# Kernel tuning notes

Hardware: AMD Instinct MI355X
Metric: run time of the kernel (lower is better)

Reference implementation:

```python
import jax, jax.numpy as jnp
import numpy as np

H = 16      # query heads
KV = 8      # kv heads
D = 128     # head_dim
HID = 2048  # hidden_size
T = 2048    # tokens
EPS = 1e-6
THETA = 1000000.0


def setup_inputs() -> dict:
    key = jax.random.key(0)
    ks = jax.random.split(key, 4)
    return {
        "hidden_states": jax.random.normal(ks[0], (T, HID), jnp.float32),
        "positions": jnp.arange(T, dtype=jnp.int32),
        "qkv_w": jax.random.normal(ks[1], (H * D + 2 * KV * D, HID), jnp.float32) * 0.02,
        "o_w": jax.random.normal(ks[2], (HID, H * D), jnp.float32) * 0.02,
        "q_norm_w": jnp.ones((D,), jnp.float32),
        "k_norm_w": jnp.ones((D,), jnp.float32),
    }


def _rmsnorm(x, w):
    # x: [T, heads, D]; normalize over last dim
    var = jnp.mean(x * x, axis=-1, keepdims=True)
    return x * jax.lax.rsqrt(var + EPS) * w


def _rope(x, positions):
    # neox-style rotate-half; x: [T, heads, D]
    half = D // 2
    inv_freq = 1.0 / (THETA ** (jnp.arange(0, half, dtype=jnp.float32) / half * 1.0))
    inv_freq = 1.0 / (THETA ** (jnp.arange(0, D, 2, dtype=jnp.float32) / D))
    ang = positions.astype(jnp.float32)[:, None] * inv_freq  # [T, D/2]
    cos = jnp.cos(ang)[:, None, :]
    sin = jnp.sin(ang)[:, None, :]
    x1, x2 = x[..., :half], x[..., half:]
    return jnp.concatenate([x1 * cos - x2 * sin, x2 * cos + x1 * sin], axis=-1)


def reference(hidden_states, positions, qkv_w, o_w, q_norm_w, k_norm_w):
    scale = D ** -0.5
    qkv = hidden_states @ qkv_w.T  # [T, H*D + 2*KV*D]
    q = qkv[:, : H * D].reshape(T, H, D)
    k = qkv[:, H * D : H * D + KV * D].reshape(T, KV, D)
    v = qkv[:, H * D + KV * D :].reshape(T, KV, D)

    q = _rope(_rmsnorm(q, q_norm_w), positions)
    k = _rope(_rmsnorm(k, k_norm_w), positions)

    # GQA: repeat kv heads to match query heads
    rep = H // KV
    k = jnp.repeat(k, rep, axis=1)  # [T, H, D]
    v = jnp.repeat(v, rep, axis=1)

    scores = jnp.einsum("thd,shd->hts", q, k) * scale  # [H, T, T]
    causal = positions[:, None] >= positions[None, :]  # [T, T]
    scores = jnp.where(causal[None, :, :], scores, jnp.float32(-1e30))
    p = jax.nn.softmax(scores, axis=-1)
    o = jnp.einsum("hts,shd->thd", p, v).reshape(T, H * D)
    return o @ o_w.T  # [T, HID]
```

## Files before the change

### kernel.cpp

```cpp
#include <hip/hip_runtime.h>
#include <math.h>

#define T_TOK 2048
#define HID 2048
#define NH 16
#define NKV 8
#define HD 128
#define QKV_N 4096
#define EPS 1e-6f

typedef unsigned short u16;
typedef unsigned int   u32;
typedef __attribute__((ext_vector_type(8))) u16   u16x8;
typedef __attribute__((ext_vector_type(8))) short short8;
typedef __attribute__((ext_vector_type(4))) float floatx4;
typedef __attribute__((ext_vector_type(4))) u32   u32x4;

__device__ __forceinline__ u16 f2bf(float x) {
    u32 u = __float_as_uint(x);
    u = (u + 0x7fffu + ((u >> 16) & 1u)) >> 16;
    return (u16)u;
}
__device__ __forceinline__ float bf2f(u16 h) {
    return __uint_as_float(((u32)h) << 16);
}

__global__ __launch_bounds__(256) void cvt_f32_bf16(
    const float* __restrict__ in, u16* __restrict__ out)
{
    const size_t i = ((size_t)blockIdx.x * 256 + threadIdx.x) * 8;
    float4 a = *(const float4*)(in + i);
    float4 b = *(const float4*)(in + i + 4);
    u16x8 o;
    o[0] = f2bf(a.x); o[1] = f2bf(a.y); o[2] = f2bf(a.z); o[3] = f2bf(a.w);
    o[4] = f2bf(b.x); o[5] = f2bf(b.y); o[6] = f2bf(b.z); o[7] = f2bf(b.w);
    *(u16x8*)(out + i) = o;
}

template<bool OUT_BF16>
__global__ __launch_bounds__(256) void gemm_bt_bf16(
    const u16* __restrict__ A, const u16* __restrict__ B,
    void* __restrict__ Cv, int K, int lda, int ldb, int ldc)
{
    __shared__ short As[128 * 32];
    __shared__ short Bs[128 * 32];

    const int tid = threadIdx.x;
    const int w   = tid >> 6;
    const int l   = tid & 63;
    const int m0  = blockIdx.y * 128;
    const int n0  = blockIdx.x * 128;
    const int wm  = (w >> 1) * 64;
    const int wn  = (w & 1) * 64;
    const int lm  = l & 15;
    const int ko8 = (l >> 4) * 8;

    const u16* gA0 = A + (size_t)(m0      + (tid >> 2)) * lda + (tid & 3) * 8;
    const u16* gA1 = A + (size_t)(m0 + 64 + (tid >> 2)) * lda + (tid & 3) * 8;
    const u16* gB0 = B + (size_t)(n0      + (tid >> 2)) * ldb + (tid & 3) * 8;
    const u16* gB1 = B + (size_t)(n0 + 64 + (tid >> 2)) * ldb + (tid & 3) * 8;
    short* lA0 = As + w * 512;
    short* lA1 = As + 2048 + w * 512;
    short* lB0 = Bs + w * 512;
    short* lB1 = Bs + 2048 + w * 512;

    floatx4 acc[4][4];
    #pragma unroll
    for (int i = 0; i < 4; ++i)
        #pragma unroll
        for (int j = 0; j < 4; ++j) acc[i][j] = (floatx4){0.f, 0.f, 0.f, 0.f};

    for (int k0 = 0; k0 < K; k0 += 32) {
        __syncthreads();
        __builtin_amdgcn_global_load_lds(
            (const __attribute__((address_space(1))) u32*)(gA0 + k0),
            (__attribute__((address_space(3))) u32*)lA0, 16, 0, 0);
        __builtin_amdgcn_global_load_lds(
            (const __attribute__((address_space(1))) u32*)(gA1 + k0),
            (__attribute__((address_space(3))) u32*)lA1, 16, 0, 0);
        __builtin_amdgcn_global_load_lds(
            (const __attribute__((address_space(1))) u32*)(gB0 + k0),
            (__attribute__((address_space(3))) u32*)lB0, 16, 0, 0);
        __builtin_amdgcn_global_load_lds(
            (const __attribute__((address_space(1))) u32*)(gB1 + k0),
            (__attribute__((address_space(3))) u32*)lB1, 16, 0, 0);
        __syncthreads();

        short8 af[4], bfr[4];
        #pragma unroll
        for (int i = 0; i < 4; ++i)
            af[i] = *(const short8*)(As + (wm + i * 16 + lm) * 32 + ko8);
        #pragma unroll
        for (int j = 0; j < 4; ++j)
            bfr[j] = *(const short8*)(Bs + (wn + j * 16 + lm) * 32 + ko8);
        #pragma unroll
        for (int i = 0; i < 4; ++i)
            #pragma unroll
            for (int j = 0; j < 4; ++j)
                acc[i][j] = __builtin_amdgcn_mfma_f32_16x16x32_bf16(
                    af[i], bfr[j], acc[i][j], 0, 0, 0);
    }

    const int r0 = (l >> 4) * 4;
    #pragma unroll
    for (int i = 0; i < 4; ++i)
        #pragma unroll
        for (int j = 0; j < 4; ++j)
            #pragma unroll
            for (int r = 0; r < 4; ++r) {
                const int row = m0 + wm + i * 16 + r0 + r;
                const int col = n0 + wn + j * 16 + lm;
                if (OUT_BF16)
                    ((u16*)Cv)[(size_t)row * ldc + col] = f2bf(acc[i][j][r]);
                else
                    ((float*)Cv)[(size_t)row * ldc + col] = acc[i][j][r];
            }
}

__global__ __launch_bounds__(128) void norm_rope(
    u16* __restrict__ qkv, const int* __restrict__ positions,
    const float* __restrict__ qw, const float* __restrict__ kw)
{
    const int t   = blockIdx.x;
    const int hh  = blockIdx.y;
    const int tid = threadIdx.x;

    u16* p; const float* w;
    if (hh < NH) { p = qkv + (size_t)t*QKV_N + hh*HD;              w = qw; }
    else         { p = qkv + (size_t)t*QKV_N + NH*HD + (hh-NH)*HD; w = kw; }

    float x = bf2f(p[tid]);

    __shared__ float red[2];
    float ss = x * x;
    #pragma unroll
    for (int o = 32; o > 0; o >>= 1) ss += __shfl_down(ss, o);
    if ((tid & 63) == 0) red[tid >> 6] = ss;
    __syncthreads();
    const float var = (red[0] + red[1]) * (1.0f / (float)HD);
    float xn = x * rsqrtf(var + EPS) * w[tid];

    __shared__ float sx[HD];
    sx[tid] = xn;
    __syncthreads();

    const int   pos = positions[t];
    const int   i   = tid & 63;
    const float inv_freq = exp2f(-(float)i * 0.311430758895690f);
    const float ang = (float)pos * inv_freq;
    const float s = sinf(ang);
    const float c = cosf(ang);

    float out;
    if (tid < 64) out = sx[i]      * c - sx[i + 64] * s;
    else          out = sx[i + 64] * c + sx[i]      * s;
    p[tid] = f2bf(out);
}

__global__ __launch_bounds__(256) void k_pack(
    const u16* __restrict__ qkv, u16* __restrict__ Kp)
{
    const int tile = blockIdx.x, kvh = blockIdx.y, tid = threadIdx.x;
    const int r  = tid >> 2;
    const int og = (tid & 3) * 4;
    const u16* src = qkv + (size_t)(tile*64 + r)*QKV_N + NH*HD + kvh*HD;
    u16* dst = Kp + ((size_t)(kvh*32 + tile)*64 + r) * 128;
    #pragma unroll
    for (int i = 0; i < 4; ++i) {
        const int o = og + i;
        *(u16x8*)(dst + o*8) = *(const u16x8*)(src + (o ^ (r & 15))*8);
    }
}

__global__ __launch_bounds__(256) void v_pack(
    const u16* __restrict__ qkv, u16* __restrict__ Vtp)
{
    const int tile = blockIdx.x, kvh = blockIdx.y, tid = threadIdx.x;
    __shared__ u16 tl[64][136];
    const int t  = tid >> 2;
    const int c0 = (tid & 3) * 32;
    const u16* src = qkv + (size_t)(tile*64 + t)*QKV_N + NH*HD + NKV*HD + kvh*HD + c0;
    #pragma unroll
    for (int p = 0; p < 4; ++p)
        *(u16x8*)(&tl[t][c0 + p*8]) = *(const u16x8*)(src + p*8);
    __syncthreads();
    u16* dstb = Vtp + (size_t)(kvh*32 + tile) * 128 * 64;
    #pragma unroll
    for (int i = 0; i < 4; ++i) {
        const int id = tid*4 + i;
        const int d = id >> 3;
        const int o = id & 7;
        const int sb = (o ^ (d & 7)) * 8;
        u16x8 v;
        #pragma unroll
        for (int j = 0; j < 8; ++j) v[j] = tl[sb + j][d];
        *(u16x8*)(dstb + d*64 + o*8) = v;
    }
}

__global__ __launch_bounds__(512) void attn_mfma(
    const u16* __restrict__ qkv, const u16* __restrict__ Kp,
    const u16* __restrict__ Vtp,
    u16* __restrict__ Opart, float2* __restrict__ ml)
{
    const int id   = blockIdx.x;
    const int half = id >> 8;
    const int kvh  = id & 7;
    const int bid  = (id & 255) >> 3;
    const int qt   = half ? bid : 31 - bid;
    const int t0   = qt * 64;
    const int tid  = threadIdx.x;
    const int w    = tid >> 6;
    const int l    = tid & 63;
    const int q4   = l >> 4;
    const int c    = l & 15;
    const int h    = kvh*2 + (w >> 2);
    const int wq   = w & 3;

    __shared__ short Ks[64 * 128];
    __shared__ short Vts[128 * 64];

    short8 bq[4];
    {
        const u16* qrow = qkv + (size_t)(t0 + wq*16 + c) * QKV_N + h*HD;
        #pragma unroll
        for (int kk = 0; kk < 4; ++kk)
            bq[kk] = *(const short8*)(qrow + kk*32 + q4*8);
    }

    float m_run = -3.0e38f, l_run = 0.f;
    floatx4 accO[8];
    #pragma unroll
    for (int db = 0; db < 8; ++db) accO[db] = (floatx4){0.f, 0.f, 0.f, 0.f};

    const float Cs = 0.12751744f;

    const int nt  = qt + 1;
    const int nh0 = (nt + 1) >> 1;
    const int tlo = half ? nh0 : 0;
    const int thi = half ? nt  : nh0;

    for (int tile = tlo; tile < thi; ++tile) {
        __syncthreads();
        {
            const size_t tb = (size_t)(kvh*32 + tile) * 8192;
            const u16* g = (w < 4 ? Kp + tb + w*2048 : Vtp + tb + (w-4)*2048) + l*8;
            short* p = (w < 4) ? (Ks + w*2048) : (Vts + (w-4)*2048);
            #pragma unroll
            for (int i = 0; i < 4; ++i)
                __builtin_amdgcn_global_load_lds(
                    (const __attribute__((address_space(1))) u32*)(g + i*512),
                    (__attribute__((address_space(3))) u32*)(p + i*512), 16, 0, 0);
        }
        __syncthreads();

        floatx4 accS[4];
        #pragma unroll
        for (int sb = 0; sb < 4; ++sb) accS[sb] = (floatx4){0.f, 0.f, 0.f, 0.f};
        #pragma unroll
        for (int kk = 0; kk < 4; ++kk) {
            #pragma unroll
            for (int sb = 0; sb < 4; ++sb) {
                short8 ak = *(const short8*)(Ks + (sb*16 + c)*128 + ((kk*4 + q4) ^ c)*8);
                accS[sb] = __builtin_amdgcn_mfma_f32_16x16x32_bf16(ak, bq[kk], accS[sb], 0, 0, 0);
            }
        }

        if (tile == qt) {
            #pragma unroll
            for (int sb = 0; sb < 4; ++sb)
                #pragma unroll
                for (int r = 0; r < 4; ++r) {
                    const int s_loc = sb*16 + q4*4 + r;
                    const int t_loc = wq*16 + c;
                    if (s_loc > t_loc) accS[sb][r] = -1.0e30f;
                }
        }

        float mt = -3.0e38f;
        #pragma unroll
        for (int sb = 0; sb < 4; ++sb)
            #pragma unroll
            for (int r = 0; r < 4; ++r) mt = fmaxf(mt, accS[sb][r]);
        mt = fmaxf(mt, __shfl_xor(mt, 16));
        mt = fmaxf(mt, __shfl_xor(mt, 32));

        const float m_new = fmaxf(m_run, mt);
        const float alpha = exp2f((m_run - m_new) * Cs);
        m_run = m_new;

        float P[4][4];
        float lsum = 0.f;
        #pragma unroll
        for (int sb = 0; sb < 4; ++sb)
            #pragma unroll
            for (int r = 0; r < 4; ++r) {
                const float e = exp2f((accS[sb][r] - m_new) * Cs);
                P[sb][r] = e;
                lsum += e;
            }
        lsum += __shfl_xor(lsum, 16);
        lsum += __shfl_xor(lsum, 32);
        l_run = l_run * alpha + lsum;

        #pragma unroll
        for (int r = 0; r < 4; ++r) {
            const float ar = __shfl(alpha, (l & 48) | (q4*4 + r));
            #pragma unroll
            for (int db = 0; db < 8; ++db) accO[db][r] *= ar;
        }

        u32 Pp[4][2];
        #pragma unroll
        for (int sb = 0; sb < 4; ++sb)
            #pragma unroll
            for (int p = 0; p < 2; ++p)
                Pp[sb][p] = (u32)f2bf(P[sb][2*p]) | ((u32)f2bf(P[sb][2*p+1]) << 16);

        const int src0 = ((2*q4    ) & 3) * 16 + c;
        const int src1 = ((2*q4 + 1) & 3) * 16 + c;
        const bool hiq = q4 >= 2;
        #pragma unroll
        for (int k2 = 0; k2 < 2; ++k2) {
            u32 x0 = __shfl(Pp[2*k2][0],   src0), y0 = __shfl(Pp[2*k2+1][0], src0);
            u32 x1 = __shfl(Pp[2*k2][1],   src0), y1 = __shfl(Pp[2*k2+1][1], src0);
            u32 x2 = __shfl(Pp[2*k2][0],   src1), y2 = __shfl(Pp[2*k2+1][0], src1);
            u32 x3 = __shfl(Pp[2*k2][1],   src1), y3 = __shfl(Pp[2*k2+1][1], src1);
            u32x4 av;
            av.x = hiq ? y0 : x0;  av.y = hiq ? y1 : x1;
            av.z = hiq ? y2 : x2;  av.w = hiq ? y3 : x3;
            const short8 aP = __builtin_bit_cast(short8, av);
            #pragma unroll
            for (int db = 0; db < 8; ++db) {
                short8 bv = *(const short8*)(Vts + (db*16 + c)*64 + (((k2*4 + q4) ^ (c & 7)))*8);
                accO[db] = __builtin_amdgcn_mfma_f32_16x16x32_bf16(aP, bv, accO[db], 0, 0, 0);
            }
        }
    }

    const size_t pbase = (size_t)(half * NH + h) * T_TOK;
    #pragma unroll
    for (int r = 0; r < 4; ++r) {
        const int qloc = q4*4 + r;
        const float mr = __shfl(m_run, (l & 48) | qloc);
        const float lr = __shfl(l_run, (l & 48) | qloc);
        const int row_g = t0 + wq*16 + qloc;
        u16* op = Opart + (pbase + row_g) * HD;
        #pragma unroll
        for (int db = 0; db < 8; ++db)
            op[db*16 + c] = f2bf(accO[db][r]);
        if (c == 0) ml[pbase + row_g] = make_float2(mr, lr);
    }
}

__global__ __launch_bounds__(256) void attn_combine(
    const u16* __restrict__ Opart, const float2* __restrict__ ml,
    u16* __restrict__ qkv)
{
    const int idx = blockIdx.x * 256 + threadIdx.x;
    const int d = idx & (HD - 1);
    const int t = (idx >> 7) & (T_TOK - 1);
    const int h = idx >> 18;
    const size_t iA = (size_t)h * T_TOK + t;
    const size_t iB = (size_t)(NH + h) * T_TOK + t;
    const float2 a = ml[iA];
    const float2 b = ml[iB];
    const float Cs = 0.12751744f;
    const float mM = fmaxf(a.x, b.x);
    const float wA = exp2f((a.x - mM) * Cs);
    const float wB = exp2f((b.x - mM) * Cs);
    const float OA = bf2f(Opart[iA * HD + d]);
    const float OB = bf2f(Opart[iB * HD + d]);
    const float o = (wA * OA + wB * OB) / (wA * a.y + wB * b.y);
    qkv[(size_t)t * QKV_N + h * HD + d] = f2bf(o);
}

extern "C" void kernel_launch(void* const* d_in, const int* in_sizes, int n_in,
                              void* d_out, int out_size, void* d_ws, size_t ws_size,
                              hipStream_t stream)
{
    const float* hidden    = (const float*)d_in[0];
    const int*   positions = (const int*)  d_in[1];
    const float* qkv_w     = (const float*)d_in[2];
    const float* o_w       = (const float*)d_in[3];
    const float* q_norm_w  = (const float*)d_in[4];
    const float* k_norm_w  = (const float*)d_in[5];
    float* out = (float*)d_out;

    u16* qkvbf = (u16*)d_ws;
    u16* wbf   = qkvbf + (size_t)T_TOK * QKV_N;
    u16* abf   = wbf   + (size_t)QKV_N * HID;
    u16* kpb   = abf   + (size_t)T_TOK * HID;
    u16* vpb   = kpb   + (size_t)NKV * T_TOK * HD;

    cvt_f32_bf16<<<(T_TOK*HID)/2048, 256, 0, stream>>>(hidden, abf);
    cvt_f32_bf16<<<(QKV_N*HID)/2048, 256, 0, stream>>>(qkv_w, wbf);

    gemm_bt_bf16<true><<<dim3(QKV_N/128, T_TOK/128), 256, 0, stream>>>(
        abf, wbf, qkvbf, HID, HID, HID, QKV_N);

    norm_rope<<<dim3(T_TOK, NH + NKV), 128, 0, stream>>>(
        qkvbf, positions, q_norm_w, k_norm_w);

    k_pack<<<dim3(T_TOK/64, NKV), 256, 0, stream>>>(qkvbf, kpb);
    v_pack<<<dim3(T_TOK/64, NKV), 256, 0, stream>>>(qkvbf, vpb);

    attn_mfma<<<512, 512, 0, stream>>>(qkvbf, kpb, vpb, wbf, (float2*)abf);

    attn_combine<<<(NH*T_TOK*HD)/256, 256, 0, stream>>>(
        wbf, (const float2*)abf, qkvbf);

    cvt_f32_bf16<<<(HID*HID)/2048, 256, 0, stream>>>(o_w, abf);
    gemm_bt_bf16<false><<<dim3(HID/128, T_TOK/128), 256, 0, stream>>>(
        qkvbf, abf, out, HID, QKV_N, HID, HID);
}
```

Measured before the change: 291.5 us.

## Fuse norm/rope with K/V packing, double-buffer attention tiles, vectorize combine

Merges the norm_rope, k_pack and v_pack kernels into one prep kernel per (64-token tile, kv head), which normalizes and rotates Q and K in registers using wave shuffles and writes rotated K straight into the swizzled packed layout. This removes two launches and one global round trip of K. The attention kernel now double-buffers the K/V tiles in LDS, issuing the next tile's async load before computing the current one, at the cost of twice the LDS per block. The combine kernel is vectorized to 8 bf16 elements per thread.

```diff
diff --git a/kernel.cpp b/kernel.cpp
--- a/kernel.cpp
+++ b/kernel.cpp
@@ -117,84 +117,86 @@
             }
 }
 
-__global__ __launch_bounds__(128) void norm_rope(
+__global__ __launch_bounds__(256) void prep(
     u16* __restrict__ qkv, const int* __restrict__ positions,
-    const float* __restrict__ qw, const float* __restrict__ kw)
-{
-    const int t   = blockIdx.x;
-    const int hh  = blockIdx.y;
+    const float* __restrict__ qw, const float* __restrict__ kw,
+    u16* __restrict__ Kp, u16* __restrict__ Vtp)
+{
+    const int tile = blockIdx.x, kvh = blockIdx.y;
     const int tid = threadIdx.x;
-
-    u16* p; const float* w;
-    if (hh < NH) { p = qkv + (size_t)t*QKV_N + hh*HD;              w = qw; }
-    else         { p = qkv + (size_t)t*QKV_N + NH*HD + (hh-NH)*HD; w = kw; }
-
-    float x = bf2f(p[tid]);
-
-    __shared__ float red[2];
-    float ss = x * x;
-    #pragma unroll
-    for (int o = 32; o > 0; o >>= 1) ss += __shfl_down(ss, o);
-    if ((tid & 63) == 0) red[tid >> 6] = ss;
+    const int w = tid >> 6, l = tid & 63;
+    const int t0 = tile * 64;
+
+    const float qw0 = qw[2*l], qw1 = qw[2*l+1];
+    const float kw0 = kw[2*l], kw1 = kw[2*l+1];
+    const int   i0  = (2*l) & 63;
+    const float if0 = exp2f(-(float)i0     * 0.311430758895690f);
+    const float if1 = exp2f(-(float)(i0+1) * 0.311430758895690f);
+
+    for (int rr = w; rr < 64; rr += 4) {
+        const int t = t0 + rr;
+        const int pos = positions[t];
+        const float a0 = (float)pos * if0;
+        const float a1 = (float)pos * if1;
+        const float s0 = sinf(a0), c0 = cosf(a0);
+        const float s1 = sinf(a1), c1 = cosf(a1);
+
+        #pragma unroll
+        for (int pass = 0; pass < 3; ++pass) {
+            const int off = (pass < 2) ? (2*kvh + pass)*HD : NH*HD + kvh*HD;
+            const float w0 = (pass < 2) ? qw0 : kw0;
+            const float w1 = (pass < 2) ? qw1 : kw1;
+            u16* p = qkv + (size_t)t*QKV_N + off;
+
+            const u32 pk = *(const u32*)(p + 2*l);
+            const float x0 = bf2f((u16)pk), x1 = bf2f((u16)(pk >> 16));
+            float ss = x0*x0 + x1*x1;
+            #pragma unroll
+            for (int x = 1; x < 64; x <<= 1) ss += __shfl_xor(ss, x);
+            const float rs = rsqrtf(ss * (1.0f/128.0f) + EPS);
+            const float xn0 = x0 * rs * w0, xn1 = x1 * rs * w1;
+            const float px0 = __shfl_xor(xn0, 32);
+            const float px1 = __shfl_xor(xn1, 32);
+
+            float o0, o1;
+            if (l < 32) { o0 = xn0*c0 - px0*s0; o1 = xn1*c1 - px1*s1; }
+            else        { o0 = xn0*c0 + px0*s0; o1 = xn1*c1 + px1*s1; }
+            const u32 outpk = (u32)f2bf(o0) | ((u32)f2bf(o1) << 16);
+
+            if (pass < 2) {
+                *(u32*)(p + 2*l) = outpk;
+            } else {
+                const int ch = l >> 2;
+                u16* dst = Kp + ((size_t)(kvh*32 + tile)*64 + rr)*128
+                              + (ch ^ (rr & 15))*8 + (l & 3)*2;
+                *(u32*)dst = outpk;
+            }
+        }
+    }
+
+    __shared__ u16 tl[64][136];
+    {
+        const int t  = tid >> 2;
+        const int c0 = (tid & 3) * 32;
+        const u16* src = qkv + (size_t)(t0 + t)*QKV_N + NH*HD + NKV*HD + kvh*HD + c0;
+        #pragma unroll
+        for (int p2 = 0; p2 < 4; ++p2)
+            *(u16x8*)(&tl[t][c0 + p2*8]) = *(const u16x8*)(src + p2*8);
+    }
     __syncthreads();
-    const float var = (red[0] + red[1]) * (1.0f / (float)HD);
-    float xn = x * rsqrtf(var + EPS) * w[tid];
-
-    __shared__ float sx[HD];
-    sx[tid] = xn;
-    __syncthreads();
-
-    const int   pos = positions[t];
-    const int   i   = tid & 63;
-    const float inv_freq = exp2f(-(float)i * 0.311430758895690f);
-    const float ang = (float)pos * inv_freq;
-    const float s = sinf(ang);
-    const float c = cosf(ang);
-
-    float out;
-    if (tid < 64) out = sx[i]      * c - sx[i + 64] * s;
-    else          out = sx[i + 64] * c + sx[i]      * s;
-    p[tid] = f2bf(out);
-}
-
-__global__ __launch_bounds__(256) void k_pack(
-    const u16* __restrict__ qkv, u16* __restrict__ Kp)
-{
-    const int tile = blockIdx.x, kvh = blockIdx.y, tid = threadIdx.x;
-    const int r  = tid >> 2;
-    const int og = (tid & 3) * 4;
-    const u16* src = qkv + (size_t)(tile*64 + r)*QKV_N + NH*HD + kvh*HD;
-    u16* dst = Kp + ((size_t)(kvh*32 + tile)*64 + r) * 128;
-    #pragma unroll
-    for (int i = 0; i < 4; ++i) {
-        const int o = og + i;
-        *(u16x8*)(dst + o*8) = *(const u16x8*)(src + (o ^ (r & 15))*8);
-    }
-}
-
-__global__ __launch_bounds__(256) void v_pack(
-    const u16* __restrict__ qkv, u16* __restrict__ Vtp)
-{
-    const int tile = blockIdx.x, kvh = blockIdx.y, tid = threadIdx.x;
-    __shared__ u16 tl[64][136];
-    const int t  = tid >> 2;
-    const int c0 = (tid & 3) * 32;
-    const u16* src = qkv + (size_t)(tile*64 + t)*QKV_N + NH*HD + NKV*HD + kvh*HD + c0;
-    #pragma unroll
-    for (int p = 0; p < 4; ++p)
-        *(u16x8*)(&tl[t][c0 + p*8]) = *(const u16x8*)(src + p*8);
-    __syncthreads();
-    u16* dstb = Vtp + (size_t)(kvh*32 + tile) * 128 * 64;
-    #pragma unroll
-    for (int i = 0; i < 4; ++i) {
-        const int id = tid*4 + i;
-        const int d = id >> 3;
-        const int o = id & 7;
-        const int sb = (o ^ (d & 7)) * 8;
-        u16x8 v;
-        #pragma unroll
-        for (int j = 0; j < 8; ++j) v[j] = tl[sb + j][d];
-        *(u16x8*)(dstb + d*64 + o*8) = v;
+    {
+        u16* dstb = Vtp + (size_t)(kvh*32 + tile) * 128 * 64;
+        #pragma unroll
+        for (int i = 0; i < 4; ++i) {
+            const int id = tid*4 + i;
+            const int d = id >> 3;
+            const int o = id & 7;
+            const int sb = (o ^ (d & 7)) * 8;
+            u16x8 v;
+            #pragma unroll
+            for (int j = 0; j < 8; ++j) v[j] = tl[sb + j][d];
+            *(u16x8*)(dstb + d*64 + o*8) = v;
+        }
     }
 }
 
@@ -217,8 +219,8 @@
     const int h    = kvh*2 + (w >> 2);
     const int wq   = w & 3;
 
-    __shared__ short Ks[64 * 128];
-    __shared__ short Vts[128 * 64];
+    __shared__ short Ks[2][64 * 128];
+    __shared__ short Vts[2][128 * 64];
 
     short8 bq[4];
     {
@@ -240,19 +242,26 @@
     const int tlo = half ? nh0 : 0;
     const int thi = half ? nt  : nh0;
 
+    auto issue = [&](int tile, int buf) {
+        const size_t tb = (size_t)(kvh*32 + tile) * 8192;
+        const u16* g = (w < 4 ? Kp + tb + w*2048 : Vtp + tb + (w-4)*2048) + l*8;
+        short* p = (w < 4) ? (Ks[buf] + w*2048) : (Vts[buf] + (w-4)*2048);
+        #pragma unroll
+        for (int i = 0; i < 4; ++i)
+            __builtin_amdgcn_global_load_lds(
+                (const __attribute__((address_space(1))) u32*)(g + i*512),
+                (__attribute__((address_space(3))) u32*)(p + i*512), 16, 0, 0);
+    };
+
+    if (tlo < thi) issue(tlo, 0);
+    int cur = 0;
+
     for (int tile = tlo; tile < thi; ++tile) {
         __syncthreads();
-        {
-            const size_t tb = (size_t)(kvh*32 + tile) * 8192;
-            const u16* g = (w < 4 ? Kp + tb + w*2048 : Vtp + tb + (w-4)*2048) + l*8;
-            short* p = (w < 4) ? (Ks + w*2048) : (Vts + (w-4)*2048);
-            #pragma unroll
-            for (int i = 0; i < 4; ++i)
-                __builtin_amdgcn_global_load_lds(
-                    (const __attribute__((address_space(1))) u32*)(g + i*512),
-                    (__attribute__((address_space(3))) u32*)(p + i*512), 16, 0, 0);
-        }
-        __syncthreads();
+        if (tile + 1 < thi) issue(tile + 1, cur ^ 1);
+
+        const short* Kc = Ks[cur];
+        const short* Vc = Vts[cur];
 
         floatx4 accS[4];
         #pragma unroll
@@ -261,7 +270,7 @@
         for (int kk = 0; kk < 4; ++kk) {
             #pragma unroll
             for (int sb = 0; sb < 4; ++sb) {
-                short8 ak = *(const short8*)(Ks + (sb*16 + c)*128 + ((kk*4 + q4) ^ c)*8);
+                short8 ak = *(const short8*)(Kc + (sb*16 + c)*128 + ((kk*4 + q4) ^ c)*8);
                 accS[sb] = __builtin_amdgcn_mfma_f32_16x16x32_bf16(ak, bq[kk], accS[sb], 0, 0, 0);
             }
         }
@@ -332,10 +341,11 @@
             const short8 aP = __builtin_bit_cast(short8, av);
             #pragma unroll
             for (int db = 0; db < 8; ++db) {
-                short8 bv = *(const short8*)(Vts + (db*16 + c)*64 + (((k2*4 + q4) ^ (c & 7)))*8);
+                short8 bv = *(const short8*)(Vc + (db*16 + c)*64 + (((k2*4 + q4) ^ (c & 7)))*8);
                 accO[db] = __builtin_amdgcn_mfma_f32_16x16x32_bf16(aP, bv, accO[db], 0, 0, 0);
             }
         }
+        cur ^= 1;
     }
 
     const size_t pbase = (size_t)(half * NH + h) * T_TOK;
@@ -358,9 +368,9 @@
     u16* __restrict__ qkv)
 {
     const int idx = blockIdx.x * 256 + threadIdx.x;
-    const int d = idx & (HD - 1);
-    const int t = (idx >> 7) & (T_TOK - 1);
-    const int h = idx >> 18;
+    const int c16 = idx & 15;
+    const int t   = (idx >> 4) & (T_TOK - 1);
+    const int h   = idx >> 15;
     const size_t iA = (size_t)h * T_TOK + t;
     const size_t iB = (size_t)(NH + h) * T_TOK + t;
     const float2 a = ml[iA];
@@ -369,10 +379,14 @@
     const float mM = fmaxf(a.x, b.x);
     const float wA = exp2f((a.x - mM) * Cs);
     const float wB = exp2f((b.x - mM) * Cs);
-    const float OA = bf2f(Opart[iA * HD + d]);
-    const float OB = bf2f(Opart[iB * HD + d]);
-    const float o = (wA * OA + wB * OB) / (wA * a.y + wB * b.y);
-    qkv[(size_t)t * QKV_N + h * HD + d] = f2bf(o);
+    const float inv = 1.0f / (wA * a.y + wB * b.y);
+    const u16x8 A = *(const u16x8*)(Opart + iA * HD + c16*8);
+    const u16x8 B = *(const u16x8*)(Opart + iB * HD + c16*8);
+    u16x8 o;
+    #pragma unroll
+    for (int j = 0; j < 8; ++j)
+        o[j] = f2bf((wA * bf2f(A[j]) + wB * bf2f(B[j])) * inv);
+    *(u16x8*)(qkv + (size_t)t * QKV_N + h * HD + c16*8) = o;
 }
 
 extern "C" void kernel_launch(void* const* d_in, const int* in_sizes, int n_in,
@@ -399,15 +413,12 @@
     gemm_bt_bf16<true><<<dim3(QKV_N/128, T_TOK/128), 256, 0, stream>>>(
         abf, wbf, qkvbf, HID, HID, HID, QKV_N);
 
-    norm_rope<<<dim3(T_TOK, NH + NKV), 128, 0, stream>>>(
-        qkvbf, positions, q_norm_w, k_norm_w);
-
-    k_pack<<<dim3(T_TOK/64, NKV), 256, 0, stream>>>(qkvbf, kpb);
-    v_pack<<<dim3(T_TOK/64, NKV), 256, 0, stream>>>(qkvbf, vpb);
+    prep<<<dim3(T_TOK/64, NKV), 256, 0, stream>>>(
+        qkvbf, positions, q_norm_w, k_norm_w, kpb, vpb);
 
     attn_mfma<<<512, 512, 0, stream>>>(qkvbf, kpb, vpb, wbf, (float2*)abf);
 
-    attn_combine<<<(NH*T_TOK*HD)/256, 256, 0, stream>>>(
+    attn_combine<<<(NH*T_TOK*16)/256, 256, 0, stream>>>(
         wbf, (const float2*)abf, qkvbf);
 
     cvt_f32_bf16<<<(HID*HID)/2048, 256, 0, stream>>>(o_w, abf);
```

Result: faster. 285.5 us (-2.1%).
